# Kernel tuning notes

Hardware: AMD Instinct MI355X
Metric: run time of the kernel (lower is better)

The kernel has to match this reference:

```python
import jax, jax.numpy as jnp
import numpy as np

HEADS = 8
NEG_SLOPE = 0.2
N_REL = 3
N_NODES = 10000
N_EDGES = 160000
OBS = 32
ACT = 8
N_GRAPHS = 16
HC = HEADS * OBS  # 256 = heads * out_channels (dim=1)


def _rgat_layer(x, w, q, k, e, we, b, src, dst, etype, eattr):
    """PyG RGATConv, additive-self-attention, across-relation, dim=1, concat=True, eval mode."""
    N = x.shape[0]
    # relation-specific transform for every node, then per-edge gather (avoids [E,in,out] bmm)
    xw = jnp.einsum('ni,rio->nro', x, w)              # [N, R, H*C]
    outi = xw[dst, etype]                              # [E, H*C] target features
    outj = xw[src, etype]                              # [E, H*C] source features
    alpha = outi @ q + outj @ k + (eattr @ we) @ e     # [E, H]
    alpha = jax.nn.leaky_relu(alpha, NEG_SLOPE)
    # segment softmax over destination neighborhoods (PyG softmax: detached max, +1e-16)
    amax = jax.lax.stop_gradient(jax.ops.segment_max(alpha, dst, num_segments=N))
    amax = jnp.where(jnp.isfinite(amax), amax, 0.0)
    ex = jnp.exp(alpha - amax[dst])
    denom = jax.ops.segment_sum(ex, dst, num_segments=N)
    attn = ex / (denom[dst] + 1e-16)                   # [E, H]
    E_ = outj.shape[0]
    msg = attn[:, :, None] * outj.reshape(E_, HEADS, -1)  # [E, H, C]
    agg = jax.ops.segment_sum(msg, dst, num_segments=N)   # [N, H, C]
    return agg.reshape(N, -1) + b                          # concat heads + bias


def setup_inputs() -> dict:
    key = jax.random.key(0)
    ks = jax.random.split(key, 32)
    s = 0.05
    inp = {
        'x': jax.random.normal(ks[0], (N_NODES, OBS), jnp.float32),
        'edge_index': jax.random.randint(ks[1], (2, N_EDGES), 0, N_NODES),
        'edge_type': jax.random.randint(ks[2], (N_EDGES,), 0, N_REL),
        'edge_attr': jax.random.normal(ks[3], (N_EDGES, 1), jnp.float32),
        'batch': jnp.sort(jax.random.randint(ks[4], (N_NODES,), 0, N_GRAPHS)),
    }
    ins = [OBS, HC, HC]
    i = 5
    for l, cin in enumerate(ins, start=1):
        inp[f'w{l}'] = s * jax.random.normal(ks[i + 0], (N_REL, cin, HC), jnp.float32)
        inp[f'q{l}'] = s * jax.random.normal(ks[i + 1], (HC, HEADS), jnp.float32)
        inp[f'k{l}'] = s * jax.random.normal(ks[i + 2], (HC, HEADS), jnp.float32)
        inp[f'e{l}'] = s * jax.random.normal(ks[i + 3], (HC, HEADS), jnp.float32)
        inp[f'we{l}'] = s * jax.random.normal(ks[i + 4], (1, HC), jnp.float32)
        inp[f'b{l}'] = jnp.zeros((HC,), jnp.float32)
        i += 5
    inp['wlin'] = s * jax.random.normal(ks[i], (HC, ACT), jnp.float32)
    inp['blin'] = jnp.zeros((ACT,), jnp.float32)
    return inp


def reference(x, edge_index, edge_type, edge_attr, batch,
              w1, q1, k1, e1, we1, b1,
              w2, q2, k2, e2, we2, b2,
              w3, q3, k3, e3, we3, b3,
              wlin, blin):
    src, dst = edge_index[0], edge_index[1]
    h = jax.nn.relu(_rgat_layer(x, w1, q1, k1, e1, we1, b1, src, dst, edge_type, edge_attr))
    h = jax.nn.relu(_rgat_layer(h, w2, q2, k2, e2, we2, b2, src, dst, edge_type, edge_attr))
    h = jax.nn.relu(_rgat_layer(h, w3, q3, k3, e3, we3, b3, src, dst, edge_type, edge_attr))
    h = jnp.tanh(h @ wlin + blin)                        # [N, ACT]
    sums = jax.ops.segment_sum(h, batch, num_segments=N_GRAPHS)
    cnts = jax.ops.segment_sum(jnp.ones((h.shape[0], 1), h.dtype), batch, num_segments=N_GRAPHS)
    return sums / jnp.maximum(cnts, 1.0)                 # global_mean_pool -> [G, ACT]
```

## Files before the change

kernel.cpp:

```cpp
#include <hip/hip_runtime.h>
#include <math.h>

#define HEADS 8
#define HC 256
#define NREL 3
#define NEG 0.2f
#define MAXDEG 64
#define NCT 17

typedef float vfloat4 __attribute__((ext_vector_type(4)));
typedef short b16x8 __attribute__((ext_vector_type(8)));
typedef float f32x4 __attribute__((ext_vector_type(4)));
typedef unsigned short u16x8 __attribute__((ext_vector_type(8)));

__device__ __forceinline__ unsigned short f2bf(float f) {
    unsigned u = __float_as_uint(f);
    unsigned r = (u + 0x7FFFu + ((u >> 16) & 1u)) >> 16;
    return (unsigned short)r;
}
__device__ __forceinline__ float bf2f(unsigned short b) {
    return __uint_as_float(((unsigned)b) << 16);
}

__global__ void k_wprep(
    const float* __restrict__ W1, const float* __restrict__ Q1, const float* __restrict__ K1,
    const float* __restrict__ E1, const float* __restrict__ WE1,
    const float* __restrict__ W2, const float* __restrict__ Q2, const float* __restrict__ K2,
    const float* __restrict__ E2, const float* __restrict__ WE2,
    const float* __restrict__ W3, const float* __restrict__ Q3, const float* __restrict__ K3,
    const float* __restrict__ E3, const float* __restrict__ WE3,
    unsigned short* __restrict__ b1hi, unsigned short* __restrict__ b1lo,
    unsigned short* __restrict__ b2hi, unsigned short* __restrict__ b2lo,
    unsigned short* __restrict__ b3hi, unsigned short* __restrict__ b3lo,
    float* __restrict__ wee,
    const int* __restrict__ ei, const int* __restrict__ et, const float* __restrict__ ea,
    int* __restrict__ fill, int2* __restrict__ bkt,
    int nnodes, int nedges, int nwcv, int nprep) {
    int bi = blockIdx.x;
    int tid = threadIdx.x;
    if (bi < nwcv) {
        const float* w;
        unsigned short *bhi, *blo;
        int K, r, kb;
        if (bi < NREL) { w = W1; bhi = b1hi; blo = b1lo; K = 32; r = bi; kb = 0; }
        else if (bi < NREL + NREL * 8) {
            int idx = bi - NREL; w = W2; bhi = b2hi; blo = b2lo; K = HC; r = idx >> 3; kb = idx & 7;
        } else {
            int idx = bi - NREL - NREL * 8; w = W3; bhi = b3hi; blo = b3lo; K = HC; r = idx >> 3; kb = idx & 7;
        }
        int KB = K / 32;
        int ct = tid >> 4, mc = tid & 15;
        int c = ct * 16 + mc;
#pragma unroll
        for (int q = 0; q < 4; ++q) {
            u16x8 hv, lv;
#pragma unroll
            for (int j = 0; j < 8; ++j) {
                float f = w[(size_t)(r * K + kb * 32 + q * 8 + j) * HC + c];
                unsigned short h = f2bf(f);
                hv[j] = h;
                lv[j] = f2bf(f - bf2f(h));
            }
            size_t base = ((((size_t)r * NCT + ct) * KB + kb) * 64 + q * 16 + mc) * 8;
            *(u16x8*)(bhi + base) = hv;
            *(u16x8*)(blo + base) = lv;
        }
        return;
    }
    bi -= nwcv;
    if (bi >= nprep) {
        int e = (bi - nprep) * 256 + tid;
        if (e < nedges) {
            int dst = ei[nedges + e];
            int pos = atomicAdd(&fill[dst], 1);
            if (pos < MAXDEG)
                bkt[dst * MAXDEG + pos] = make_int2((ei[e] << 2) | (et[e] & 3),
                                                    __float_as_int(ea[e]));
        }
        return;
    }
    {
        int w = tid >> 5, lane = tid & 31;
        int row = bi * 8 + w;
        const float *wmat, *qm, *km, *em, *wem;
        unsigned short *bhi, *blo;
        int K, layer, lbi;
        if (row < NREL * 32) {
            layer = 0; lbi = row; K = 32;
            wmat = W1; qm = Q1; km = K1; em = E1; wem = WE1; bhi = b1hi; blo = b1lo;
        } else if (row < NREL * 32 + NREL * HC) {
            layer = 1; lbi = row - NREL * 32; K = HC;
            wmat = W2; qm = Q2; km = K2; em = E2; wem = WE2; bhi = b2hi; blo = b2lo;
        } else {
            layer = 2; lbi = row - NREL * 32 - NREL * HC; K = HC;
            wmat = W3; qm = Q3; km = K3; em = E3; wem = WE3; bhi = b3hi; blo = b3lo;
        }
        int r = lbi / K, i = lbi - r * K;
        int KB = K / 32;
        int kb = i >> 5, qq = (i >> 3) & 3, j = i & 7;
        const float* wrow = wmat + (size_t)lbi * HC;
        float pq[8] = {0.f, 0.f, 0.f, 0.f, 0.f, 0.f, 0.f, 0.f};
        float pk[8] = {0.f, 0.f, 0.f, 0.f, 0.f, 0.f, 0.f, 0.f};
#pragma unroll
        for (int it = 0; it < HC; it += 32) {
            int o = it + lane;
            float wv = wrow[o];
            float4 qa = *(const float4*)(qm + (size_t)o * 8);
            float4 qb = *(const float4*)(qm + (size_t)o * 8 + 4);
            float4 ka = *(const float4*)(km + (size_t)o * 8);
            float4 kc = *(const float4*)(km + (size_t)o * 8 + 4);
            pq[0] += wv * qa.x; pq[1] += wv * qa.y; pq[2] += wv * qa.z; pq[3] += wv * qa.w;
            pq[4] += wv * qb.x; pq[5] += wv * qb.y; pq[6] += wv * qb.z; pq[7] += wv * qb.w;
            pk[0] += wv * ka.x; pk[1] += wv * ka.y; pk[2] += wv * ka.z; pk[3] += wv * ka.w;
            pk[4] += wv * kc.x; pk[5] += wv * kc.y; pk[6] += wv * kc.z; pk[7] += wv * kc.w;
        }
#pragma unroll
        for (int off = 16; off > 0; off >>= 1) {
#pragma unroll
            for (int u = 0; u < 8; ++u) {
                pq[u] += __shfl_xor(pq[u], off, 32);
                pk[u] += __shfl_xor(pk[u], off, 32);
            }
        }
        size_t base = (((size_t)r * NCT + 16) * KB + kb) * 512 + j;
        if (lane < 16) {
            int h = lane & 7;
            bool isq = lane < 8;
            float v;
            switch (h) {
                case 0: v = isq ? pq[0] : pk[0]; break;
                case 1: v = isq ? pq[1] : pk[1]; break;
                case 2: v = isq ? pq[2] : pk[2]; break;
                case 3: v = isq ? pq[3] : pk[3]; break;
                case 4: v = isq ? pq[4] : pk[4]; break;
                case 5: v = isq ? pq[5] : pk[5]; break;
                case 6: v = isq ? pq[6] : pk[6]; break;
                default: v = isq ? pq[7] : pk[7]; break;
            }
            size_t o = base + (size_t)(qq * 16 + (isq ? 0 : 8) + h) * 8;
            unsigned short hh = f2bf(v);
            bhi[o] = hh;
            blo[o] = f2bf(v - bf2f(hh));
        }
        if (lbi == 0 && w == 0 && lane < HEADS) {
            float s = 0.f;
            for (int o = 0; o < HC; o++) s += wem[o] * em[o * HEADS + lane];
            wee[layer * HEADS + lane] = s;
        }
        return;
    }
}

template <int K, int NT, bool RAWX>
__global__ __launch_bounds__(256) void k_mfma(const unsigned short* __restrict__ pahi,
                                              const unsigned short* __restrict__ palo,
                                              const unsigned short* __restrict__ pbhi,
                                              const unsigned short* __restrict__ pblo,
                                              const float* __restrict__ xraw,
                                              float* __restrict__ xw,
                                              float* __restrict__ qdot,
                                              float* __restrict__ kdot,
                                              int nnodes, int ntiles) {
    constexpr int KB = K / 32;
    int ntg = blockIdx.x;
    int r = blockIdx.y;
    int t = threadIdx.x;
    int wv = t >> 6, lane = t & 63;
    int q = lane >> 4, m = lane & 15;
    f32x4 acc[5][NT] = {};
    for (int kb = 0; kb < KB; ++kb) {
        b16x8 ah[NT], al[NT];
#pragma unroll
        for (int ti = 0; ti < NT; ++ti) {
            int nt = ntg * NT + ti;
            if (nt >= ntiles) nt = ntiles - 1;
            if constexpr (RAWX) {
                int row = nt * 16 + m;
                if (row >= nnodes) row = nnodes - 1;
                const float4* xr = (const float4*)(xraw + (size_t)row * 32 + q * 8);
                float4 f0 = xr[0], f1 = xr[1];
                float fv[8] = {f0.x, f0.y, f0.z, f0.w, f1.x, f1.y, f1.z, f1.w};
#pragma unroll
                for (int j = 0; j < 8; ++j) {
                    unsigned short hh = f2bf(fv[j]);
                    ah[ti][j] = (short)hh;
                    al[ti][j] = (short)f2bf(fv[j] - bf2f(hh));
                }
            } else {
                size_t ao = (((size_t)nt * KB + kb) * 64 + lane) * 8;
                ah[ti] = *(const b16x8*)(pahi + ao);
                al[ti] = *(const b16x8*)(palo + ao);
            }
        }
#pragma unroll
        for (int s = 0; s < 5; ++s) {
            int ct = wv + 4 * s;
            if (ct >= NCT) continue;
            size_t o = (((size_t)r * NCT + ct) * KB + kb) * 512 + (size_t)lane * 8;
            b16x8 vbh = *(const b16x8*)(pbhi + o);
            b16x8 vbl = *(const b16x8*)(pblo + o);
#pragma unroll
            for (int ti = 0; ti < NT; ++ti) {
                acc[s][ti] = __builtin_amdgcn_mfma_f32_16x16x32_bf16(ah[ti], vbh, acc[s][ti], 0, 0, 0);
                acc[s][ti] = __builtin_amdgcn_mfma_f32_16x16x32_bf16(al[ti], vbh, acc[s][ti], 0, 0, 0);
                acc[s][ti] = __builtin_amdgcn_mfma_f32_16x16x32_bf16(ah[ti], vbl, acc[s][ti], 0, 0, 0);
            }
        }
    }
#pragma unroll
    for (int ti = 0; ti < NT; ++ti) {
        int nt = ntg * NT + ti;
        if (nt >= ntiles) continue;
        int n0 = nt * 16;
#pragma unroll
        for (int s = 0; s < 5; ++s) {
            int ct = wv + 4 * s;
            if (ct >= NCT) continue;
            if (ct < 16) {
                int c = ct * 16 + m;
#pragma unroll
                for (int g = 0; g < 4; ++g) {
                    int n = n0 + q * 4 + g;
                    if (n < nnodes) xw[((size_t)n * NREL + r) * HC + c] = acc[s][ti][g];
                }
            } else {
#pragma unroll
                for (int g = 0; g < 4; ++g) {
                    int n = n0 + q * 4 + g;
                    if (n < nnodes) {
                        if (m < 8) qdot[n * 24 + r * 8 + m] = acc[s][ti][g];
                        else       kdot[n * 24 + r * 8 + (m - 8)] = acc[s][ti][g];
                    }
                }
            }
        }
    }
}

__global__ __launch_bounds__(256) void k_agg(const float* __restrict__ xw,
                      const float* __restrict__ qdot, const float* __restrict__ kdot,
                      const int* __restrict__ fill, const int2* __restrict__ bkt,
                      const float* __restrict__ wee,
                      const float* __restrict__ bias,
                      unsigned short* __restrict__ houthi, unsigned short* __restrict__ houtlo,
                      float* __restrict__ out8,
                      const float* __restrict__ wlin, const float* __restrict__ blin,
                      int nnodes) {
    __shared__ float salpha[4][MAXDEG * HEADS];
    __shared__ int spack[4][MAXDEG];
    int wv = threadIdx.x >> 6, lane = threadIdx.x & 63;
    int n = blockIdx.x * 4 + wv;
    if (n >= nnodes) return;
    int beg = n * MAXDEG;
    int deg = fill[n];
    if (deg > MAXDEG) deg = MAXDEG;
    float* sal = salpha[wv];
    int* spk = spack[wv];
    {
        int h = lane & 7;
        float weeh = wee[h];
        const float* qdn = qdot + n * 24;
        for (int base = 0; base < deg; base += 8) {
            int d = base + (lane >> 3);
            if (d < deg) {
                int2 pa = bkt[beg + d];
                int pk = pa.x;
                float ae = __int_as_float(pa.y);
                int s = pk >> 2, t = pk & 3;
                if (h == 0) spk[d] = pk;
                float a = qdn[t * 8 + h] + kdot[s * 24 + t * 8 + h] + ae * weeh;
                sal[d * 8 + h] = (a > 0.f) ? a : NEG * a;
            }
        }
    }
    float sinv_h;
    {
        int h = lane & 7, c = lane >> 3;
        float m = -INFINITY;
        for (int d = c; d < deg; d += 8) m = fmaxf(m, sal[d * 8 + h]);
        m = fmaxf(m, __shfl_xor(m, 8, 64));
        m = fmaxf(m, __shfl_xor(m, 16, 64));
        m = fmaxf(m, __shfl_xor(m, 32, 64));
        float s = 0.f;
        for (int d = c; d < deg; d += 8) {
            float ex = expf(sal[d * 8 + h] - m);
            sal[d * 8 + h] = ex;
            s += ex;
        }
        s += __shfl_xor(s, 8, 64);
        s += __shfl_xor(s, 16, 64);
        s += __shfl_xor(s, 32, 64);
        sinv_h = 1.f / (s + 1e-16f);
    }
    float sinv_sel = __shfl(sinv_h, lane >> 3, 64);
    int hsel = lane >> 3;
    float4 acc4 = make_float4(0.f, 0.f, 0.f, 0.f);
    int d = 0;
    for (; d + 7 < deg; d += 8) {
        const float4* rp[8];
        float av[8];
#pragma unroll
        for (int u = 0; u < 8; ++u) {
            int pk = spk[d + u];
            rp[u] = (const float4*)(xw + ((size_t)(pk >> 2) * NREL + (pk & 3)) * HC);
            av[u] = sal[(d + u) * 8 + hsel];
        }
        float4 vv[8];
#pragma unroll
        for (int u = 0; u < 8; ++u) vv[u] = rp[u][lane];
#pragma unroll
        for (int u = 0; u < 8; ++u) {
            acc4.x += av[u] * vv[u].x;
            acc4.y += av[u] * vv[u].y;
            acc4.z += av[u] * vv[u].z;
            acc4.w += av[u] * vv[u].w;
        }
    }
    for (; d + 3 < deg; d += 4) {
        int pk0 = spk[d], pk1 = spk[d + 1], pk2 = spk[d + 2], pk3 = spk[d + 3];
        const float4* r0 = (const float4*)(xw + ((size_t)(pk0 >> 2) * NREL + (pk0 & 3)) * HC);
        const float4* r1 = (const float4*)(xw + ((size_t)(pk1 >> 2) * NREL + (pk1 & 3)) * HC);
        const float4* r2 = (const float4*)(xw + ((size_t)(pk2 >> 2) * NREL + (pk2 & 3)) * HC);
        const float4* r3 = (const float4*)(xw + ((size_t)(pk3 >> 2) * NREL + (pk3 & 3)) * HC);
        float4 v0 = r0[lane], v1 = r1[lane], v2 = r2[lane], v3 = r3[lane];
        float a0 = sal[d * 8 + hsel];
        float a1 = sal[(d + 1) * 8 + hsel];
        float a2 = sal[(d + 2) * 8 + hsel];
        float a3 = sal[(d + 3) * 8 + hsel];
        acc4.x += a0 * v0.x + a1 * v1.x + a2 * v2.x + a3 * v3.x;
        acc4.y += a0 * v0.y + a1 * v1.y + a2 * v2.y + a3 * v3.y;
        acc4.z += a0 * v0.z + a1 * v1.z + a2 * v2.z + a3 * v3.z;
        acc4.w += a0 * v0.w + a1 * v1.w + a2 * v2.w + a3 * v3.w;
    }
    for (; d < deg; ++d) {
        int pk = spk[d];
        const float4* r0 = (const float4*)(xw + ((size_t)(pk >> 2) * NREL + (pk & 3)) * HC);
        float4 v0 = r0[lane];
        float a0 = sal[d * 8 + hsel];
        acc4.x += a0 * v0.x;
        acc4.y += a0 * v0.y;
        acc4.z += a0 * v0.z;
        acc4.w += a0 * v0.w;
    }
    float4 bv = *(const float4*)(bias + lane * 4);
    float vv4[4];
    vv4[0] = fmaxf(acc4.x * sinv_sel + bv.x, 0.f);
    vv4[1] = fmaxf(acc4.y * sinv_sel + bv.y, 0.f);
    vv4[2] = fmaxf(acc4.z * sinv_sel + bv.z, 0.f);
    vv4[3] = fmaxf(acc4.w * sinv_sel + bv.w, 0.f);
    if (houthi) {
        int ntile = n >> 4, mm = n & 15;
#pragma unroll
        for (int i = 0; i < 4; ++i) {
            int c = lane * 4 + i;
            int kb = c >> 5, q = (c >> 3) & 3, j = c & 7;
            size_t o2 = ((((size_t)ntile * 8 + kb) * 64) + q * 16 + mm) * 8 + j;
            unsigned short hh = f2bf(vv4[i]);
            houthi[o2] = hh;
            houtlo[o2] = f2bf(vv4[i] - bf2f(hh));
        }
    }
    if (out8) {
        float part[8] = {0.f, 0.f, 0.f, 0.f, 0.f, 0.f, 0.f, 0.f};
#pragma unroll
        for (int i = 0; i < 4; ++i) {
            const float4* wr = (const float4*)(wlin + (size_t)(lane * 4 + i) * 8);
            float4 wa = wr[0], wb = wr[1];
            float vi = vv4[i];
            part[0] += vi * wa.x; part[1] += vi * wa.y;
            part[2] += vi * wa.z; part[3] += vi * wa.w;
            part[4] += vi * wb.x; part[5] += vi * wb.y;
            part[6] += vi * wb.z; part[7] += vi * wb.w;
        }
#pragma unroll
        for (int off = 32; off > 0; off >>= 1) {
#pragma unroll
            for (int u = 0; u < 8; ++u) part[u] += __shfl_xor(part[u], off, 64);
        }
        if (lane < 8) {
            float sel;
            switch (lane) {
                case 0: sel = part[0]; break;
                case 1: sel = part[1]; break;
                case 2: sel = part[2]; break;
                case 3: sel = part[3]; break;
                case 4: sel = part[4]; break;
                case 5: sel = part[5]; break;
                case 6: sel = part[6]; break;
                default: sel = part[7]; break;
            }
            out8[(size_t)n * 8 + lane] = tanhf(sel + blin[lane]);
        }
    }
}

__global__ __launch_bounds__(256) void k_pool8(const float* __restrict__ out8,
                                               const int* __restrict__ batch,
                                               float* __restrict__ out, int nnodes) {
    int g = blockIdx.x;
    __shared__ int sb[2];
    __shared__ float sred[256];
    if (threadIdx.x < 2) {
        int target = g + threadIdx.x;
        int lo = 0, hi = nnodes;
        while (lo < hi) { int mid = (lo + hi) >> 1; if (batch[mid] < target) lo = mid + 1; else hi = mid; }
        sb[threadIdx.x] = lo;
    }
    __syncthreads();
    int beg = sb[0], end = sb[1];
    int t = threadIdx.x, h = t & 7, c = t >> 3;
    float s0 = 0.f, s1 = 0.f, s2 = 0.f, s3 = 0.f;
    int i = beg + c;
    for (; i + 96 < end; i += 128) {
        s0 += out8[(size_t)i * 8 + h];
        s1 += out8[(size_t)(i + 32) * 8 + h];
        s2 += out8[(size_t)(i + 64) * 8 + h];
        s3 += out8[(size_t)(i + 96) * 8 + h];
    }
    for (; i < end; i += 32) s0 += out8[(size_t)i * 8 + h];
    sred[t] = (s0 + s1) + (s2 + s3);
    __syncthreads();
    if (t < 8) {
        float a = 0.f;
        for (int j = 0; j < 32; ++j) a += sred[t + 8 * j];
        out[g * 8 + t] = a / fmaxf((float)(end - beg), 1.f);
    }
}


extern "C" void kernel_launch(void* const* d_in, const int* in_sizes, int n_in,
                              void* d_out, int out_size, void* d_ws, size_t ws_size,
                              hipStream_t stream) {
    const float* x    = (const float*)d_in[0];
    const int*   ei   = (const int*)d_in[1];
    const int*   et   = (const int*)d_in[2];
    const float* ea   = (const float*)d_in[3];
    const int*   batch = (const int*)d_in[4];
    const float* W[3]  = {(const float*)d_in[5],  (const float*)d_in[11], (const float*)d_in[17]};
    const float* Q[3]  = {(const float*)d_in[6],  (const float*)d_in[12], (const float*)d_in[18]};
    const float* K[3]  = {(const float*)d_in[7],  (const float*)d_in[13], (const float*)d_in[19]};
    const float* Em[3] = {(const float*)d_in[8],  (const float*)d_in[14], (const float*)d_in[20]};
    const float* WE[3] = {(const float*)d_in[9],  (const float*)d_in[15], (const float*)d_in[21]};
    const float* B[3]  = {(const float*)d_in[10], (const float*)d_in[16], (const float*)d_in[22]};
    const float* wlin = (const float*)d_in[23];
    const float* blin = (const float*)d_in[24];

    int nnodes = in_sizes[0] / 32;
    int nedges = in_sizes[2];
    int ngraph = 16;
    int npad = (nnodes + 15) & ~15;
    int ntiles = npad / 16;

    char* ws = (char*)d_ws;
    size_t off = 0;
    auto alloc = [&](size_t bytes) -> void* {
        void* p = ws + off;
        off = (off + bytes + 255) & ~(size_t)255;
        return p;
    };
    int*   fill     = (int*)alloc((size_t)(nnodes + 64) * 4);
    int2*  bkt      = (int2*)alloc((size_t)nnodes * MAXDEG * 8);
    float* xw       = (float*)alloc((size_t)npad * NREL * HC * 4);
    float* qdot     = (float*)alloc((size_t)npad * NREL * HEADS * 4);
    float* kdot     = (float*)alloc((size_t)npad * NREL * HEADS * 4);
    float* wee      = (float*)alloc((size_t)NREL * HEADS * 4);
    float* out8     = (float*)alloc((size_t)npad * 8 * 4);
    unsigned short* hahi = (unsigned short*)alloc((size_t)npad * HC * 2);
    unsigned short* halo = (unsigned short*)alloc((size_t)npad * HC * 2);
    unsigned short* hbhi = (unsigned short*)alloc((size_t)npad * HC * 2);
    unsigned short* hblo = (unsigned short*)alloc((size_t)npad * HC * 2);
    unsigned short* wt1hi = (unsigned short*)alloc((size_t)NREL * NCT * 1 * 512 * 2);
    unsigned short* wt1lo = (unsigned short*)alloc((size_t)NREL * NCT * 1 * 512 * 2);
    unsigned short* wt2hi = (unsigned short*)alloc((size_t)NREL * NCT * 8 * 512 * 2);
    unsigned short* wt2lo = (unsigned short*)alloc((size_t)NREL * NCT * 8 * 512 * 2);
    unsigned short* wt3hi = (unsigned short*)alloc((size_t)NREL * NCT * 8 * 512 * 2);
    unsigned short* wt3lo = (unsigned short*)alloc((size_t)NREL * NCT * 8 * 512 * 2);
    (void)ws_size; (void)n_in; (void)out_size;

    int nwcv = NREL * (1 + 8 + 8);
    int nprep = (NREL * 32 + 2 * NREL * HC) / 8;
    int nscat = (nedges + 255) / 256;

    hipMemsetAsync(fill, 0, (size_t)(nnodes + 64) * 4, stream);
    k_wprep<<<nwcv + nprep + nscat, 256, 0, stream>>>(
        W[0], Q[0], K[0], Em[0], WE[0],
        W[1], Q[1], K[1], Em[1], WE[1],
        W[2], Q[2], K[2], Em[2], WE[2],
        wt1hi, wt1lo, wt2hi, wt2lo, wt3hi, wt3lo, wee,
        ei, et, ea, fill, bkt,
        nnodes, nedges, nwcv, nprep);

    dim3 gmfma((ntiles + 1) / 2, NREL);
    int gagg = (nnodes + 3) / 4;

    k_mfma<32, 2, true><<<gmfma, 256, 0, stream>>>(nullptr, nullptr, wt1hi, wt1lo, x,
                                                   xw, qdot, kdot, nnodes, ntiles);
    k_agg<<<gagg, 256, 0, stream>>>(xw, qdot, kdot, fill, bkt, wee + 0, B[0],
                                    hahi, halo, nullptr, nullptr, nullptr, nnodes);

    k_mfma<HC, 2, false><<<gmfma, 256, 0, stream>>>(hahi, halo, wt2hi, wt2lo, nullptr,
                                                    xw, qdot, kdot, nnodes, ntiles);
    k_agg<<<gagg, 256, 0, stream>>>(xw, qdot, kdot, fill, bkt, wee + 8, B[1],
                                    hbhi, hblo, nullptr, nullptr, nullptr, nnodes);

    k_mfma<HC, 2, false><<<gmfma, 256, 0, stream>>>(hbhi, hblo, wt3hi, wt3lo, nullptr,
                                                    xw, qdot, kdot, nnodes, ntiles);
    k_agg<<<gagg, 256, 0, stream>>>(xw, qdot, kdot, fill, bkt, wee + 16, B[2],
                                    nullptr, nullptr, out8, wlin, blin, nnodes);

    k_pool8<<<ngraph, 256, 0, stream>>>(out8, batch, (float*)d_out, nnodes);
}
```

Measured before the change: 292.2 us.

## Prefetch neighbor rows ahead of softmax and double-buffer aggregation loads

Alpha computation now gives each lane one edge and uses float4 loads of qdot/kdot/wee instead of the 8-lanes-per-edge layout. The first batch of eight gathered xw rows is issued before the softmax reduction so its latency overlaps that work. The main aggregation loop then ping-pongs between two register buffers, loading the next eight rows while accumulating the current ones. This raises register pressure, which may lower occupancy, and it relies on there being no barrier between the shared-memory writes and reads, which is fine within a single wavefront.

```diff
diff --git a/kernel.cpp b/kernel.cpp
--- a/kernel.cpp
+++ b/kernel.cpp
@@ -256,22 +256,43 @@
     if (deg > MAXDEG) deg = MAXDEG;
     float* sal = salpha[wv];
     int* spk = spack[wv];
-    {
-        int h = lane & 7;
-        float weeh = wee[h];
-        const float* qdn = qdot + n * 24;
-        for (int base = 0; base < deg; base += 8) {
-            int d = base + (lane >> 3);
-            if (d < deg) {
-                int2 pa = bkt[beg + d];
-                int pk = pa.x;
-                float ae = __int_as_float(pa.y);
-                int s = pk >> 2, t = pk & 3;
-                if (h == 0) spk[d] = pk;
-                float a = qdn[t * 8 + h] + kdot[s * 24 + t * 8 + h] + ae * weeh;
-                sal[d * 8 + h] = (a > 0.f) ? a : NEG * a;
-            }
-        }
+    if (lane < deg) {
+        int2 pa = bkt[beg + lane];
+        int pk = pa.x;
+        float ae = __int_as_float(pa.y);
+        int s = pk >> 2, t = pk & 3;
+        spk[lane] = pk;
+        float4 q0 = *(const float4*)(qdot + n * 24 + t * 8);
+        float4 q1 = *(const float4*)(qdot + n * 24 + t * 8 + 4);
+        float4 k0 = *(const float4*)(kdot + s * 24 + t * 8);
+        float4 k1 = *(const float4*)(kdot + s * 24 + t * 8 + 4);
+        float4 w0 = *(const float4*)(wee);
+        float4 w1 = *(const float4*)(wee + 4);
+        float a0 = q0.x + k0.x + ae * w0.x;
+        float a1 = q0.y + k0.y + ae * w0.y;
+        float a2 = q0.z + k0.z + ae * w0.z;
+        float a3 = q0.w + k0.w + ae * w0.w;
+        float a4 = q1.x + k1.x + ae * w1.x;
+        float a5 = q1.y + k1.y + ae * w1.y;
+        float a6 = q1.z + k1.z + ae * w1.z;
+        float a7 = q1.w + k1.w + ae * w1.w;
+        a0 = (a0 > 0.f) ? a0 : NEG * a0;
+        a1 = (a1 > 0.f) ? a1 : NEG * a1;
+        a2 = (a2 > 0.f) ? a2 : NEG * a2;
+        a3 = (a3 > 0.f) ? a3 : NEG * a3;
+        a4 = (a4 > 0.f) ? a4 : NEG * a4;
+        a5 = (a5 > 0.f) ? a5 : NEG * a5;
+        a6 = (a6 > 0.f) ? a6 : NEG * a6;
+        a7 = (a7 > 0.f) ? a7 : NEG * a7;
+        *(float4*)(sal + lane * 8) = make_float4(a0, a1, a2, a3);
+        *(float4*)(sal + lane * 8 + 4) = make_float4(a4, a5, a6, a7);
+    }
+#define ROWP(pkv) ((const float4*)(xw + ((size_t)((pkv) >> 2) * NREL + ((pkv) & 3)) * HC))
+    float4 vA[8], vB[8];
+    int nb8 = deg >> 3;
+    if (nb8 >= 1) {
+#pragma unroll
+        for (int u = 0; u < 8; ++u) vA[u] = ROWP(spk[u])[lane];
     }
     float sinv_h;
     {
@@ -296,32 +317,48 @@
     int hsel = lane >> 3;
     float4 acc4 = make_float4(0.f, 0.f, 0.f, 0.f);
     int d = 0;
-    for (; d + 7 < deg; d += 8) {
-        const float4* rp[8];
-        float av[8];
-#pragma unroll
-        for (int u = 0; u < 8; ++u) {
-            int pk = spk[d + u];
-            rp[u] = (const float4*)(xw + ((size_t)(pk >> 2) * NREL + (pk & 3)) * HC);
-            av[u] = sal[(d + u) * 8 + hsel];
-        }
-        float4 vv[8];
-#pragma unroll
-        for (int u = 0; u < 8; ++u) vv[u] = rp[u][lane];
-#pragma unroll
-        for (int u = 0; u < 8; ++u) {
-            acc4.x += av[u] * vv[u].x;
-            acc4.y += av[u] * vv[u].y;
-            acc4.z += av[u] * vv[u].z;
-            acc4.w += av[u] * vv[u].w;
+#define CONS(buf, base)                                                        \
+    {                                                                          \
+        _Pragma("unroll") for (int u = 0; u < 8; ++u) {                        \
+            float av = sal[((base) + u) * 8 + hsel];                           \
+            acc4.x += av * buf[u].x;                                           \
+            acc4.y += av * buf[u].y;                                           \
+            acc4.z += av * buf[u].z;                                           \
+            acc4.w += av * buf[u].w;                                           \
+        }                                                                      \
+    }
+    if (nb8 >= 1) {
+        for (;;) {
+            int dn = d + 8;
+            if (dn + 8 <= deg) {
+#pragma unroll
+                for (int u = 0; u < 8; ++u) vB[u] = ROWP(spk[dn + u])[lane];
+                CONS(vA, d);
+                d = dn;
+                int dn2 = d + 8;
+                if (dn2 + 8 <= deg) {
+#pragma unroll
+                    for (int u = 0; u < 8; ++u) vA[u] = ROWP(spk[dn2 + u])[lane];
+                    CONS(vB, d);
+                    d = dn2;
+                } else {
+                    CONS(vB, d);
+                    d = dn2;
+                    break;
+                }
+            } else {
+                CONS(vA, d);
+                d = dn;
+                break;
+            }
         }
     }
     for (; d + 3 < deg; d += 4) {
         int pk0 = spk[d], pk1 = spk[d + 1], pk2 = spk[d + 2], pk3 = spk[d + 3];
-        const float4* r0 = (const float4*)(xw + ((size_t)(pk0 >> 2) * NREL + (pk0 & 3)) * HC);
-        const float4* r1 = (const float4*)(xw + ((size_t)(pk1 >> 2) * NREL + (pk1 & 3)) * HC);
-        const float4* r2 = (const float4*)(xw + ((size_t)(pk2 >> 2) * NREL + (pk2 & 3)) * HC);
-        const float4* r3 = (const float4*)(xw + ((size_t)(pk3 >> 2) * NREL + (pk3 & 3)) * HC);
+        const float4* r0 = ROWP(pk0);
+        const float4* r1 = ROWP(pk1);
+        const float4* r2 = ROWP(pk2);
+        const float4* r3 = ROWP(pk3);
         float4 v0 = r0[lane], v1 = r1[lane], v2 = r2[lane], v3 = r3[lane];
         float a0 = sal[d * 8 + hsel];
         float a1 = sal[(d + 1) * 8 + hsel];
@@ -334,7 +371,7 @@
     }
     for (; d < deg; ++d) {
         int pk = spk[d];
-        const float4* r0 = (const float4*)(xw + ((size_t)(pk >> 2) * NREL + (pk & 3)) * HC);
+        const float4* r0 = ROWP(pk);
         float4 v0 = r0[lane];
         float a0 = sal[d * 8 + hsel];
         acc4.x += a0 * v0.x;
@@ -342,6 +379,8 @@
         acc4.z += a0 * v0.z;
         acc4.w += a0 * v0.w;
     }
+#undef CONS
+#undef ROWP
     float4 bv = *(const float4*)(bias + lane * 4);
     float vv4[4];
     vv4[0] = fmaxf(acc4.x * sinv_sel + bv.x, 0.f);
```

New measurement: 292.5 us, median of 2. No clear change (+0.1%).
